# Kernel tuning notes

Measured on AMD Instinct MI355X. Metric: run time of the kernel, lower is better.

Reference implementation:

```python
import jax, jax.numpy as jnp
import numpy as np

# Module dims (match init_kwargs)
D_IN = 1024
N_PRI = 2048
D_PRI = 16
N_CLS = 25
D_CLS = 16
ITERS = 3
B = 64
EPS = 1e-6


def layer_norm(x, g, b, eps=1e-5):
    m = x.mean(-1, keepdims=True)
    v = ((x - m) ** 2).mean(-1, keepdims=True)
    return (x - m) / jnp.sqrt(v + eps) * g + b


def setup_inputs() -> dict:
    key = jax.random.key(0)
    ks = jax.random.split(key, 6)
    s = lambda n: 1.0 / np.sqrt(n)
    return {
        "z": jax.random.normal(ks[0], (B, D_IN), jnp.float32),
        # to_primary: Linear(d_in, n_primary*d_primary)
        "w1": jax.random.normal(ks[1], (D_IN, N_PRI * D_PRI), jnp.float32) * s(D_IN),
        "b1": jnp.zeros((N_PRI * D_PRI,), jnp.float32),
        # primary_act: LayerNorm(d_in) -> Linear(d_in, n_primary) -> Sigmoid
        "ln1_g": jnp.ones((D_IN,), jnp.float32),
        "ln1_b": jnp.zeros((D_IN,), jnp.float32),
        "w2": jax.random.normal(ks[2], (D_IN, N_PRI), jnp.float32) * s(D_IN),
        "b2": jnp.zeros((N_PRI,), jnp.float32),
        # CapsuleFC transform + EM routing params
        "w_caps": jax.random.normal(ks[3], (N_PRI, D_PRI, N_CLS, D_CLS), jnp.float32) * s(D_PRI),
        "beta_u": jnp.zeros((N_CLS,), jnp.float32),
        "beta_a": jnp.zeros((N_CLS,), jnp.float32),
        # to_logits: LayerNorm(d_class) -> Linear(d_class, 1)
        "ln2_g": jnp.ones((D_CLS,), jnp.float32),
        "ln2_b": jnp.zeros((D_CLS,), jnp.float32),
        "w3": jax.random.normal(ks[4], (D_CLS, 1), jnp.float32) * s(D_CLS),
        "b3": jnp.zeros((1,), jnp.float32),
    }


def em_routing(V, a_in, beta_u, beta_a, n_iter):
    # V: (b, n_in, n_out, d) votes; a_in: (b, n_in) primary activations
    b, n, o, d = V.shape
    R = jnp.full((b, n, o), 1.0 / o, V.dtype)  # routing assignments
    lam = jnp.asarray(1.0, V.dtype)            # inverse temperature
    for _ in range(n_iter):
        # M-step: weighted mean/variance per output capsule
        r = R * a_in[:, :, None]                                  # (b,n,o)
        r_sum = r.sum(axis=1) + EPS                               # (b,o)
        mu = jnp.einsum('bno,bnod->bod', r, V) / r_sum[..., None]  # (b,o,d)
        diff2 = (V - mu[:, None]) ** 2                            # (b,n,o,d)
        sigma2 = jnp.einsum('bno,bnod->bod', r, diff2) / r_sum[..., None] + EPS
        cost = (beta_u[None, :, None] + 0.5 * jnp.log(sigma2)) * r_sum[..., None]
        a_out = jax.nn.sigmoid(lam * (beta_a[None, :] - cost.sum(-1)))  # (b,o)
        # E-step: Gaussian log-likelihood of each vote under each output capsule
        logp = (-0.5 * (diff2 / sigma2[:, None]).sum(-1)
                - 0.5 * jnp.log(sigma2).sum(-1)[:, None, :])      # (b,n,o)
        R = jax.nn.softmax(jnp.log(a_out + EPS)[:, None, :] + logp, axis=-1)
    return mu, a_out, R


def reference(z, w1, b1, ln1_g, ln1_b, w2, b2, w_caps, beta_u, beta_a,
              ln2_g, ln2_b, w3, b3):
    b = z.shape[0]
    # primary poses (no squash: use_squash_primary=False)
    primary_pose = (z @ w1 + b1).reshape(b, N_PRI, D_PRI)
    # primary activations
    primary_act = jnp.clip(jax.nn.sigmoid(layer_norm(z, ln1_g, ln1_b) @ w2 + b2), 0.0, 1.0)
    # votes: each primary capsule predicts each class capsule's pose
    V = jnp.einsum('bni,niod->bnod', primary_pose, w_caps)  # (B, N_PRI, N_CLS, D_CLS)
    class_pose, class_act, q = em_routing(V, primary_act, beta_u, beta_a, ITERS)
    logits = (layer_norm(class_pose, ln2_g, ln2_b) @ w3 + b3).squeeze(-1)  # (B, N_CLS)
    acts = jnp.linalg.norm(class_pose, axis=-1)                            # (B, N_CLS)
    return logits, acts, class_pose, q
```

## Files before the change

### kernel.cpp

```cpp
#include <hip/hip_runtime.h>
#include <hip/hip_bf16.h>
#include <cstdio>

#define B     64
#define DIN   1024
#define NPRI  2048
#define DPRI  16
#define NCLS  25
#define DCLS  16
#define EMEPS 1e-6f
#define LNEPS 1e-5f
#define KS2   8
#define NCH   16

#define OFF_POSE 0
#define OFF_ZN   (OFF_POSE + NPRI*DPRI*B)
#define OFF_ACTT (OFF_ZN + B*DIN)
#define OFF_G2P  (OFF_ACTT + NPRI*B)
#define OFF_V    (OFF_G2P + KS2*NPRI*B)
#define V_FLOATS (NPRI*NCLS*B*DCLS/2)
#define OFF_R    (OFF_V + V_FLOATS)
#define R_FLOATS (NPRI*NCLS*B/2)
#define OFF_PART (OFF_R + R_FLOATS)
#define OFF_MU   (OFF_PART + NCLS*NCH*33*B)
#define OFF_MI4  (OFF_MU + NCLS*DCLS*B)
#define OFF_BASE (OFF_MI4 + NCLS*8*B*4)
#define OFF_ZH   (OFF_BASE + NCLS*B)
#define WS_FLOATS (OFF_ZH + B*DIN/2)

typedef __attribute__((ext_vector_type(8))) _Float16 f16x8;
typedef __attribute__((ext_vector_type(4))) float f32x4;

__device__ __forceinline__ unsigned pack_f16(float a, float b) {
  union { _Float16 h[2]; unsigned u; } x;
  x.h[0] = (_Float16)a; x.h[1] = (_Float16)b;
  return x.u;
}
__device__ __forceinline__ float f16lo(unsigned u) {
  union { unsigned u; _Float16 h[2]; } x; x.u = u; return (float)x.h[0];
}
__device__ __forceinline__ float f16hi(unsigned u) {
  union { unsigned u; _Float16 h[2]; } x; x.u = u; return (float)x.h[1];
}
__device__ __forceinline__ unsigned short f16bits(float a) {
  union { _Float16 h; unsigned short u; } x; x.h = (_Float16)a; return x.u;
}
__device__ __forceinline__ float f16val(unsigned short u) {
  union { unsigned short u; _Float16 h; } x; x.u = u; return (float)x.h;
}

__global__ __launch_bounds__(256) void k_lnzh(const float* __restrict__ z,
                                              const float* __restrict__ g,
                                              const float* __restrict__ bb,
                                              float* __restrict__ zn,
                                              unsigned* __restrict__ zh) {
  int row = blockIdx.x, t = threadIdx.x;
  const float* zr = z + row * DIN;
  float4 v = ((const float4*)zr)[t];
  uint2 hz = {pack_f16(v.x, v.y), pack_f16(v.z, v.w)};
  *(uint2*)&zh[row * 512 + t * 2] = hz;
  float s  = v.x + v.y + v.z + v.w;
  float s2 = v.x*v.x + v.y*v.y + v.z*v.z + v.w*v.w;
  for (int off = 32; off; off >>= 1) {
    s  += __shfl_down(s, off);
    s2 += __shfl_down(s2, off);
  }
  __shared__ float ls[8];
  int wv = t >> 6, ln = t & 63;
  if (ln == 0) { ls[wv*2] = s; ls[wv*2+1] = s2; }
  __syncthreads();
  s  = ls[0] + ls[2] + ls[4] + ls[6];
  s2 = ls[1] + ls[3] + ls[5] + ls[7];
  float mean = s * (1.0f / DIN);
  float var  = s2 * (1.0f / DIN) - mean * mean;
  float inv  = 1.0f / sqrtf(var + LNEPS);
  float4 gg = ((const float4*)g)[t];
  float4 bv = ((const float4*)bb)[t];
  float4 o;
  o.x = (v.x - mean) * inv * gg.x + bv.x;
  o.y = (v.y - mean) * inv * gg.y + bv.y;
  o.z = (v.z - mean) * inv * gg.z + bv.z;
  o.w = (v.w - mean) * inv * gg.w + bv.w;
  ((float4*)(zn + row * DIN))[t] = o;
}

__global__ __launch_bounds__(512) void k_gemm1m(const unsigned* __restrict__ zh,
                                                const float* __restrict__ w1,
                                                const float* __restrict__ b1,
                                                float* __restrict__ poseT) {
  __shared__ __align__(16) unsigned bt[2][64 * 68];
  __shared__ __align__(16) unsigned zl[2][64 * 68];
  int t = threadIdx.x;
  int c0 = blockIdx.x * 64;
  int l = t & 63, w = t >> 6;
  int kh = w >> 2, cw = w & 3;
  int c15 = l & 15, kq = l >> 4;
  int h  = t >> 8;
  int th = t & 255;
  int s_kp = th >> 2;
  int s_q  = th & 3;

  f32x4 acc0 = {0,0,0,0}, acc1 = {0,0,0,0}, acc2 = {0,0,0,0}, acc3 = {0,0,0,0};

  for (int it = 0; it < 4; ++it) {
    int k0 = (h * 4 + it) * 128;
#pragma unroll
    for (int u = 0; u < 4; ++u) {
      int cq = s_q + 4 * u;
      const float* src0 = w1 + (size_t)(k0 + 2 * s_kp) * 32768 + c0 + cq * 4;
      float4 r0 = *(const float4*)src0;
      float4 r1 = *(const float4*)(src0 + 32768);
      unsigned* dst = &bt[h][(cq * 4) * 68 + s_kp];
      dst[0]   = pack_f16(r0.x, r1.x);
      dst[68]  = pack_f16(r0.y, r1.y);
      dst[136] = pack_f16(r0.z, r1.z);
      dst[204] = pack_f16(r0.w, r1.w);
    }
#pragma unroll
    for (int u = 0; u < 4; ++u) {
      int ku4 = s_q + 4 * u;
      uint4 v = *(const uint4*)&zh[(size_t)s_kp * 512 + (k0 >> 1) + ku4 * 4];
      *(uint4*)&zl[h][s_kp * 68 + ku4 * 4] = v;
    }
    __syncthreads();
#pragma unroll
    for (int ks = 0; ks < 4; ++ks) {
      union { uint4 u; f16x8 hh; } bf, a0, a1, a2, a3;
      bf.u = *(const uint4*)&bt[kh][(cw * 16 + c15) * 68 + ks * 16 + kq * 4];
      a0.u = *(const uint4*)&zl[kh][(c15)      * 68 + ks * 16 + kq * 4];
      a1.u = *(const uint4*)&zl[kh][(16 + c15) * 68 + ks * 16 + kq * 4];
      a2.u = *(const uint4*)&zl[kh][(32 + c15) * 68 + ks * 16 + kq * 4];
      a3.u = *(const uint4*)&zl[kh][(48 + c15) * 68 + ks * 16 + kq * 4];
      acc0 = __builtin_amdgcn_mfma_f32_16x16x32_f16(a0.hh, bf.hh, acc0, 0, 0, 0);
      acc1 = __builtin_amdgcn_mfma_f32_16x16x32_f16(a1.hh, bf.hh, acc1, 0, 0, 0);
      acc2 = __builtin_amdgcn_mfma_f32_16x16x32_f16(a2.hh, bf.hh, acc2, 0, 0, 0);
      acc3 = __builtin_amdgcn_mfma_f32_16x16x32_f16(a3.hh, bf.hh, acc3, 0, 0, 0);
    }
    __syncthreads();
  }

  float* red = (float*)&zl[0][0];
  if (kh == 1) {
    int cc = cw * 16 + c15;
    *(float4*)&red[cc * 68 + kq * 4]      = *(float4*)&acc0;
    *(float4*)&red[cc * 68 + 16 + kq * 4] = *(float4*)&acc1;
    *(float4*)&red[cc * 68 + 32 + kq * 4] = *(float4*)&acc2;
    *(float4*)&red[cc * 68 + 48 + kq * 4] = *(float4*)&acc3;
  }
  __syncthreads();
  if (kh == 0) {
    int cc = cw * 16 + c15;
    int c = c0 + cc;
    float bc = b1[c];
    float4 r0 = *(float4*)&red[cc * 68 + kq * 4];
    float4 r1 = *(float4*)&red[cc * 68 + 16 + kq * 4];
    float4 r2 = *(float4*)&red[cc * 68 + 32 + kq * 4];
    float4 r3 = *(float4*)&red[cc * 68 + 48 + kq * 4];
    float* pdst = poseT + (size_t)c * 64 + kq * 4;
    float4 o0 = {acc0[0] + r0.x + bc, acc0[1] + r0.y + bc, acc0[2] + r0.z + bc, acc0[3] + r0.w + bc};
    float4 o1 = {acc1[0] + r1.x + bc, acc1[1] + r1.y + bc, acc1[2] + r1.z + bc, acc1[3] + r1.w + bc};
    float4 o2 = {acc2[0] + r2.x + bc, acc2[1] + r2.y + bc, acc2[2] + r2.z + bc, acc2[3] + r2.w + bc};
    float4 o3 = {acc3[0] + r3.x + bc, acc3[1] + r3.y + bc, acc3[2] + r3.z + bc, acc3[3] + r3.w + bc};
    *(float4*)&pdst[0]  = o0;
    *(float4*)&pdst[16] = o1;
    *(float4*)&pdst[32] = o2;
    *(float4*)&pdst[48] = o3;
  }
}

__global__ __launch_bounds__(256, 2) void k_gemm2p(const float* __restrict__ zn,
                                                   const float* __restrict__ w2,
                                                   float* __restrict__ part) {
  __shared__ __align__(16) float znT[128 * 68];
  __shared__ __align__(16) float wl[128 * 68];
  int t = threadIdx.x;
  int c0 = blockIdx.x * 64;
  int k0 = blockIdx.y * 128;
  int zr_ = t >> 2, za = t & 3;
  int wk = t >> 1, wc = (t & 1) * 32;

#pragma unroll
  for (int jj = 0; jj < 4; ++jj) {
    int kb = za * 8 + jj * 32;
    const float* src = zn + zr_ * DIN + k0 + kb;
    float4 v0 = *(const float4*)src;
    float4 v1 = *(const float4*)(src + 4);
    znT[(kb+0)*68 + zr_] = v0.x; znT[(kb+1)*68 + zr_] = v0.y;
    znT[(kb+2)*68 + zr_] = v0.z; znT[(kb+3)*68 + zr_] = v0.w;
    znT[(kb+4)*68 + zr_] = v1.x; znT[(kb+5)*68 + zr_] = v1.y;
    znT[(kb+6)*68 + zr_] = v1.z; znT[(kb+7)*68 + zr_] = v1.w;
  }
  const float* wsrc = w2 + (size_t)(k0 + wk) * NPRI + c0 + wc;
#pragma unroll
  for (int j = 0; j < 8; ++j)
    *(float4*)&wl[wk * 68 + wc + j * 4] = *(const float4*)(wsrc + j * 4);
  __syncthreads();

  int r0 = (t >> 4) * 4, c0l = (t & 15) * 4;
  float acc[4][4];
#pragma unroll
  for (int j = 0; j < 4; ++j)
#pragma unroll
    for (int i = 0; i < 4; ++i) acc[j][i] = 0.f;

#pragma unroll 4
  for (int k = 0; k < 128; ++k) {
    float4 z4 = *(const float4*)&znT[k * 68 + r0];
    float4 w4 = *(const float4*)&wl[k * 68 + c0l];
    float zz[4] = {z4.x, z4.y, z4.z, z4.w};
    float ww[4] = {w4.x, w4.y, w4.z, w4.w};
#pragma unroll
    for (int j = 0; j < 4; ++j)
#pragma unroll
      for (int i = 0; i < 4; ++i) acc[j][i] += ww[j] * zz[i];
  }
  float* pdst = part + ((size_t)blockIdx.y * NPRI + c0 + c0l) * 64 + r0;
#pragma unroll
  for (int j = 0; j < 4; ++j) {
    float4 o = {acc[j][0], acc[j][1], acc[j][2], acc[j][3]};
    *(float4*)&pdst[j * 64] = o;
  }
}

__global__ __launch_bounds__(256) void k_gemm2r(const float* __restrict__ part,
                                                const float* __restrict__ b2,
                                                float* __restrict__ actt) {
  int idx = blockIdx.x * 256 + threadIdx.x;
  float4 s = {0.f, 0.f, 0.f, 0.f};
#pragma unroll
  for (int kz = 0; kz < KS2; ++kz) {
    float4 v = *(const float4*)&part[(size_t)kz * NPRI * 64 + idx * 4];
    s.x += v.x; s.y += v.y; s.z += v.z; s.w += v.w;
  }
  int c = (idx * 4) >> 6;
  float bc = b2[c];
  float4 o;
  o.x = fminf(fmaxf(1.0f / (1.0f + expf(-(s.x + bc))), 0.0f), 1.0f);
  o.y = fminf(fmaxf(1.0f / (1.0f + expf(-(s.y + bc))), 0.0f), 1.0f);
  o.z = fminf(fmaxf(1.0f / (1.0f + expf(-(s.z + bc))), 0.0f), 1.0f);
  o.w = fminf(fmaxf(1.0f / (1.0f + expf(-(s.w + bc))), 0.0f), 1.0f);
  *(float4*)&actt[idx * 4] = o;
}

__global__ __launch_bounds__(256) void k_votes(const float* __restrict__ poseT,
                                               const float* __restrict__ wcaps,
                                               unsigned* __restrict__ V) {
  __shared__ __align__(16) float wl[6400];
  __shared__ __align__(16) float pl[64 * 16];
  int n = blockIdx.x, t = threadIdx.x;
  const float* wsrc = wcaps + (size_t)n * 6400;
  for (int idx = t * 4; idx < 6400; idx += 1024)
    *(float4*)(wl + idx) = *(const float4*)(wsrc + idx);
  {
    float4 v = *(const float4*)(poseT + n * 1024 + t * 4);
    int i = (t * 4) >> 6, b = (t * 4) & 63;
    pl[(b+0)*16 + i] = v.x; pl[(b+1)*16 + i] = v.y;
    pl[(b+2)*16 + i] = v.z; pl[(b+3)*16 + i] = v.w;
  }
  __syncthreads();
  if (t >= 200) return;
  int o = t / 8, d0 = (t % 8) * 2;
  float w0[16], w1_[16];
#pragma unroll
  for (int i = 0; i < 16; ++i) {
    w0[i]  = wl[(i * 25 + o) * 16 + d0];
    w1_[i] = wl[(i * 25 + o) * 16 + d0 + 1];
  }
  unsigned* vd = V + (((size_t)n * 25 + o) * 64 * 16 + d0) / 2;
  for (int b = 0; b < 64; ++b) {
    const float* pb = &pl[b * 16];
    float a0 = 0.f, a1 = 0.f;
#pragma unroll
    for (int i = 0; i < 16; ++i) {
      float p = pb[i];
      a0 += p * w0[i];
      a1 += p * w1_[i];
    }
    vd[b * 8] = pack_f16(a0, a1);
  }
}

template <bool UNIFORM>
__global__ __launch_bounds__(256) void k_stats(const unsigned* __restrict__ V,
                                               const float* __restrict__ actt,
                                               const unsigned short* __restrict__ Rh,
                                               float* __restrict__ part) {
  int o = blockIdx.y;
  int t = threadIdx.x, b = t & 63, wv = t >> 6;
  float S0 = 0.f, S1[16], S2[16];
#pragma unroll
  for (int d = 0; d < 16; ++d) { S1[d] = 0.f; S2[d] = 0.f; }
  int n0 = blockIdx.x * 128 + wv * 32;
  for (int k = 0; k < 32; ++k) {
    int n = n0 + k;
    float a = actt[n * 64 + b];
    float r = UNIFORM ? a * (1.0f / 25.0f)
                      : f16val(Rh[((size_t)n * 25 + o) * 64 + b]) * a;
    const uint4* vp = (const uint4*)(V + (((size_t)n * 25 + o) * 64 + b) * 8);
    uint4 u0 = vp[0], u1 = vp[1];
    unsigned uu[8] = {u0.x, u0.y, u0.z, u0.w, u1.x, u1.y, u1.z, u1.w};
    S0 += r;
#pragma unroll
    for (int q = 0; q < 8; ++q) {
      float v0 = f16lo(uu[q]), v1 = f16hi(uu[q]);
      float t0 = r * v0, t1 = r * v1;
      S1[2*q]   += t0;          S1[2*q+1] += t1;
      S2[2*q]   += t0 * v0;     S2[2*q+1] += t1 * v1;
    }
  }
  __shared__ float red[4 * 33 * 64];
  red[(wv * 33 + 0) * 64 + b] = S0;
#pragma unroll
  for (int d = 0; d < 16; ++d) {
    red[(wv * 33 + 1 + d) * 64 + b]  = S1[d];
    red[(wv * 33 + 17 + d) * 64 + b] = S2[d];
  }
  __syncthreads();
  if (wv == 0) {
    for (int s = 0; s < 33; ++s) {
      float tot = red[s * 64 + b] + red[(33 + s) * 64 + b] +
                  red[(66 + s) * 64 + b] + red[(99 + s) * 64 + b];
      part[((o * NCH + blockIdx.x) * 33 + s) * 64 + b] = tot;
    }
  }
}

template <bool FINAL>
__global__ __launch_bounds__(256) void k_redfin(const float* __restrict__ part,
                                                const float* __restrict__ beta_u,
                                                const float* __restrict__ beta_a,
                                                float* __restrict__ mi4,
                                                float* __restrict__ basew,
                                                const float* __restrict__ g2,
                                                const float* __restrict__ bb2,
                                                const float* __restrict__ w3,
                                                const float* __restrict__ b3,
                                                float* __restrict__ out) {
  __shared__ float st[33 * 64];
  int o = blockIdx.x, t = threadIdx.x;
  for (int slot = t; slot < 33 * 64; slot += 256) {
    float s = 0.f;
    const float* pp = part + (size_t)o * NCH * 2112 + slot;
#pragma unroll
    for (int c = 0; c < NCH; ++c) s += pp[(size_t)c * 2112];
    st[slot] = s;
  }
  __syncthreads();
  if (t < 64) {
    int b = t;
    float s0 = st[b];
    float rsm = s0 + EMEPS;
    float inv_rs = 1.0f / rsm;
    float ldet = 0.f;
    float mloc[16], iloc[16];
#pragma unroll
    for (int d = 0; d < 16; ++d) {
      float s1 = st[(1 + d) * 64 + b];
      float s2 = st[(17 + d) * 64 + b];
      float m = s1 * inv_rs;
      float var = (s2 - 2.0f * m * s1 + m * m * s0) * inv_rs;
      float sg = fmaxf(var, 0.0f) + EMEPS;
      mloc[d] = m;
      iloc[d] = 1.0f / sg;
      ldet += logf(sg);
    }
#pragma unroll
    for (int q = 0; q < 8; ++q) {
      float4 v = {mloc[2*q], iloc[2*q], mloc[2*q+1], iloc[2*q+1]};
      *(float4*)&mi4[((o * 8 + q) * 64 + b) * 4] = v;
    }
    float cost = (16.0f * beta_u[o] + 0.5f * ldet) * rsm;
    float x = beta_a[o] - cost;
    float a = 1.0f / (1.0f + expf(-x));
    basew[o * 64 + b] = logf(a + EMEPS) - 0.5f * ldet;

    if (FINAL) {
      float sm = 0.f;
#pragma unroll
      for (int d = 0; d < 16; ++d) sm += mloc[d];
      float mean = sm * (1.0f / 16.0f);
      float var2 = 0.f;
#pragma unroll
      for (int d = 0; d < 16; ++d) { float dd = mloc[d] - mean; var2 += dd * dd; }
      var2 *= (1.0f / 16.0f);
      float inv2 = 1.0f / sqrtf(var2 + LNEPS);
      float logit = 0.f, nrm = 0.f;
#pragma unroll
      for (int d = 0; d < 16; ++d) {
        float nh = (mloc[d] - mean) * inv2 * g2[d] + bb2[d];
        logit += nh * w3[d];
        nrm += mloc[d] * mloc[d];
      }
      out[b * 25 + o] = logit + b3[0];
      out[1600 + b * 25 + o] = sqrtf(nrm);
      float* pp = out + 3200 + (b * 25 + o) * 16;
#pragma unroll
      for (int d = 0; d < 16; ++d) pp[d] = mloc[d];
    }
  }
}

template <bool FINAL>
__global__ __launch_bounds__(256) void k_estep(const unsigned* __restrict__ V,
                                               const float* __restrict__ mi4,
                                               const float* __restrict__ basew,
                                               unsigned short* __restrict__ Rh,
                                               float* __restrict__ qout) {
  int t = threadIdx.x, b = t & 63, ng = t >> 6;
  int n = blockIdx.x * 4 + ng;
  float l[25];
  float mx = -1e30f;
#pragma unroll
  for (int o = 0; o < 25; ++o) {
    const uint4* vp = (const uint4*)(V + (((size_t)n * 25 + o) * 64 + b) * 8);
    uint4 u0 = vp[0], u1 = vp[1];
    unsigned uu[8] = {u0.x, u0.y, u0.z, u0.w, u1.x, u1.y, u1.z, u1.w};
    float acc = 0.f;
#pragma unroll
    for (int qq = 0; qq < 8; ++qq) {
      float4 mi = *(const float4*)&mi4[((o * 8 + qq) * 64 + b) * 4];
      float d0 = f16lo(uu[qq]) - mi.x;
      float d1 = f16hi(uu[qq]) - mi.z;
      acc += d0 * d0 * mi.y + d1 * d1 * mi.w;
    }
    l[o] = basew[o * 64 + b] - 0.5f * acc;
    mx = fmaxf(mx, l[o]);
  }
  float s = 0.f;
#pragma unroll
  for (int o = 0; o < 25; ++o) { l[o] = expf(l[o] - mx); s += l[o]; }
  float inv = 1.0f / s;
  if (FINAL) {
    float* qp = qout + ((size_t)b * NPRI + n) * 25;
#pragma unroll
    for (int o = 0; o < 25; ++o) qp[o] = l[o] * inv;
  } else {
#pragma unroll
    for (int o = 0; o < 25; ++o)
      Rh[((size_t)n * 25 + o) * 64 + b] = f16bits(l[o] * inv);
  }
}

extern "C" void kernel_launch(void* const* d_in, const int* in_sizes, int n_in,
                              void* d_out, int out_size, void* d_ws, size_t ws_size,
                              hipStream_t stream) {
  const float* z      = (const float*)d_in[0];
  const float* w1     = (const float*)d_in[1];
  const float* b1     = (const float*)d_in[2];
  const float* ln1g   = (const float*)d_in[3];
  const float* ln1b   = (const float*)d_in[4];
  const float* w2     = (const float*)d_in[5];
  const float* b2     = (const float*)d_in[6];
  const float* wcaps  = (const float*)d_in[7];
  const float* beta_u = (const float*)d_in[8];
  const float* beta_a = (const float*)d_in[9];
  const float* ln2g   = (const float*)d_in[10];
  const float* ln2b   = (const float*)d_in[11];
  const float* w3     = (const float*)d_in[12];
  const float* b3     = (const float*)d_in[13];

  if (ws_size < (size_t)WS_FLOATS * 4) {
    fprintf(stderr, "kernel_launch: ws too small: %zu < %zu bytes\n",
            ws_size, (size_t)WS_FLOATS * 4);
  }

  float* ws    = (float*)d_ws;
  float* out   = (float*)d_out;
  float* poseT = ws + OFF_POSE;
  float* zn    = ws + OFF_ZN;
  float* actt  = ws + OFF_ACTT;
  float* g2p   = ws + OFF_G2P;
  unsigned* V  = (unsigned*)(ws + OFF_V);
  unsigned short* Rh = (unsigned short*)(ws + OFF_R);
  float* part  = ws + OFF_PART;
  float* mi4   = ws + OFF_MI4;
  float* bse   = ws + OFF_BASE;
  unsigned* zh = (unsigned*)(ws + OFF_ZH);

  k_lnzh<<<64, 256, 0, stream>>>(z, ln1g, ln1b, zn, zh);
  k_gemm1m<<<512, 512, 0, stream>>>(zh, w1, b1, poseT);
  k_gemm2p<<<dim3(32, KS2), 256, 0, stream>>>(zn, w2, g2p);
  k_gemm2r<<<128, 256, 0, stream>>>(g2p, b2, actt);
  k_votes<<<2048, 256, 0, stream>>>(poseT, wcaps, V);

  k_stats<true><<<dim3(NCH, 25), 256, 0, stream>>>(V, actt, Rh, part);
  k_redfin<false><<<25, 256, 0, stream>>>(part, beta_u, beta_a, mi4, bse,
                                          ln2g, ln2b, w3, b3, out);

  k_estep<false><<<512, 256, 0, stream>>>(V, mi4, bse, Rh, nullptr);
  k_stats<false><<<dim3(NCH, 25), 256, 0, stream>>>(V, actt, Rh, part);
  k_redfin<false><<<25, 256, 0, stream>>>(part, beta_u, beta_a, mi4, bse,
                                          ln2g, ln2b, w3, b3, out);

  k_estep<false><<<512, 256, 0, stream>>>(V, mi4, bse, Rh, nullptr);
  k_stats<false><<<dim3(NCH, 25), 256, 0, stream>>>(V, actt, Rh, part);
  k_redfin<true><<<25, 256, 0, stream>>>(part, beta_u, beta_a, mi4, bse,
                                         ln2g, ln2b, w3, b3, out);

  k_estep<true><<<512, 256, 0, stream>>>(V, mi4, bse, nullptr, out + 28800);
}
```

Baseline: 350.0 us.

## Split GEMM1 K-halves across blocks and fold partial sum and bias into votes

The first projection GEMM moves from one 512-thread block that reduces two K-halves in shared memory to two 256-thread blocks per column tile, one per K-half, each writing its own partial pose buffer. The votes kernel then adds the two partials plus the bias while staging poses into shared memory. This doubles the number of blocks and halves shared memory per block to raise occupancy and parallelism on the weight-streaming GEMM, and drops the in-block reduction. In exchange it writes and reads an extra pose-sized partial buffer in global memory.

```diff
diff --git a/kernel.cpp b/kernel.cpp
--- a/kernel.cpp
+++ b/kernel.cpp
@@ -14,7 +14,7 @@
 #define NCH   16
 
 #define OFF_POSE 0
-#define OFF_ZN   (OFF_POSE + NPRI*DPRI*B)
+#define OFF_ZN   (OFF_POSE + 2*NPRI*DPRI*B)
 #define OFF_ACTT (OFF_ZN + B*DIN)
 #define OFF_G2P  (OFF_ACTT + NPRI*B)
 #define OFF_V    (OFF_G2P + KS2*NPRI*B)
@@ -22,8 +22,7 @@
 #define OFF_R    (OFF_V + V_FLOATS)
 #define R_FLOATS (NPRI*NCLS*B/2)
 #define OFF_PART (OFF_R + R_FLOATS)
-#define OFF_MU   (OFF_PART + NCLS*NCH*33*B)
-#define OFF_MI4  (OFF_MU + NCLS*DCLS*B)
+#define OFF_MI4  (OFF_PART + NCLS*NCH*33*B)
 #define OFF_BASE (OFF_MI4 + NCLS*8*B*4)
 #define OFF_ZH   (OFF_BASE + NCLS*B)
 #define WS_FLOATS (OFF_ZH + B*DIN/2)
@@ -84,33 +83,31 @@
   ((float4*)(zn + row * DIN))[t] = o;
 }
 
-__global__ __launch_bounds__(512) void k_gemm1m(const unsigned* __restrict__ zh,
+__global__ __launch_bounds__(256) void k_gemm1m(const unsigned* __restrict__ zh,
                                                 const float* __restrict__ w1,
-                                                const float* __restrict__ b1,
-                                                float* __restrict__ poseT) {
-  __shared__ __align__(16) unsigned bt[2][64 * 68];
-  __shared__ __align__(16) unsigned zl[2][64 * 68];
+                                                float* __restrict__ poseP) {
+  __shared__ __align__(16) unsigned bt[64 * 68];
+  __shared__ __align__(16) unsigned zl[64 * 68];
   int t = threadIdx.x;
   int c0 = blockIdx.x * 64;
-  int l = t & 63, w = t >> 6;
-  int kh = w >> 2, cw = w & 3;
+  int kh = blockIdx.y;
+  int l = t & 63, cw = t >> 6;
   int c15 = l & 15, kq = l >> 4;
-  int h  = t >> 8;
-  int th = t & 255;
-  int s_kp = th >> 2;
-  int s_q  = th & 3;
+  int s_kp = t >> 2;
+  int s_q  = t & 3;
 
   f32x4 acc0 = {0,0,0,0}, acc1 = {0,0,0,0}, acc2 = {0,0,0,0}, acc3 = {0,0,0,0};
 
   for (int it = 0; it < 4; ++it) {
-    int k0 = (h * 4 + it) * 128;
+    int k0 = (kh * 4 + it) * 128;
+    if (it) __syncthreads();
 #pragma unroll
     for (int u = 0; u < 4; ++u) {
       int cq = s_q + 4 * u;
       const float* src0 = w1 + (size_t)(k0 + 2 * s_kp) * 32768 + c0 + cq * 4;
       float4 r0 = *(const float4*)src0;
       float4 r1 = *(const float4*)(src0 + 32768);
-      unsigned* dst = &bt[h][(cq * 4) * 68 + s_kp];
+      unsigned* dst = &bt[(cq * 4) * 68 + s_kp];
       dst[0]   = pack_f16(r0.x, r1.x);
       dst[68]  = pack_f16(r0.y, r1.y);
       dst[136] = pack_f16(r0.z, r1.z);
@@ -120,52 +117,30 @@
     for (int u = 0; u < 4; ++u) {
       int ku4 = s_q + 4 * u;
       uint4 v = *(const uint4*)&zh[(size_t)s_kp * 512 + (k0 >> 1) + ku4 * 4];
-      *(uint4*)&zl[h][s_kp * 68 + ku4 * 4] = v;
+      *(uint4*)&zl[s_kp * 68 + ku4 * 4] = v;
     }
     __syncthreads();
 #pragma unroll
     for (int ks = 0; ks < 4; ++ks) {
       union { uint4 u; f16x8 hh; } bf, a0, a1, a2, a3;
-      bf.u = *(const uint4*)&bt[kh][(cw * 16 + c15) * 68 + ks * 16 + kq * 4];
-      a0.u = *(const uint4*)&zl[kh][(c15)      * 68 + ks * 16 + kq * 4];
-      a1.u = *(const uint4*)&zl[kh][(16 + c15) * 68 + ks * 16 + kq * 4];
-      a2.u = *(const uint4*)&zl[kh][(32 + c15) * 68 + ks * 16 + kq * 4];
-      a3.u = *(const uint4*)&zl[kh][(48 + c15) * 68 + ks * 16 + kq * 4];
+      bf.u = *(const uint4*)&bt[(cw * 16 + c15) * 68 + ks * 16 + kq * 4];
+      a0.u = *(const uint4*)&zl[(c15)      * 68 + ks * 16 + kq * 4];
+      a1.u = *(const uint4*)&zl[(16 + c15) * 68 + ks * 16 + kq * 4];
+      a2.u = *(const uint4*)&zl[(32 + c15) * 68 + ks * 16 + kq * 4];
+      a3.u = *(const uint4*)&zl[(48 + c15) * 68 + ks * 16 + kq * 4];
       acc0 = __builtin_amdgcn_mfma_f32_16x16x32_f16(a0.hh, bf.hh, acc0, 0, 0, 0);
       acc1 = __builtin_amdgcn_mfma_f32_16x16x32_f16(a1.hh, bf.hh, acc1, 0, 0, 0);
       acc2 = __builtin_amdgcn_mfma_f32_16x16x32_f16(a2.hh, bf.hh, acc2, 0, 0, 0);
       acc3 = __builtin_amdgcn_mfma_f32_16x16x32_f16(a3.hh, bf.hh, acc3, 0, 0, 0);
     }
-    __syncthreads();
-  }
-
-  float* red = (float*)&zl[0][0];
-  if (kh == 1) {
-    int cc = cw * 16 + c15;
-    *(float4*)&red[cc * 68 + kq * 4]      = *(float4*)&acc0;
-    *(float4*)&red[cc * 68 + 16 + kq * 4] = *(float4*)&acc1;
-    *(float4*)&red[cc * 68 + 32 + kq * 4] = *(float4*)&acc2;
-    *(float4*)&red[cc * 68 + 48 + kq * 4] = *(float4*)&acc3;
-  }
-  __syncthreads();
-  if (kh == 0) {
-    int cc = cw * 16 + c15;
-    int c = c0 + cc;
-    float bc = b1[c];
-    float4 r0 = *(float4*)&red[cc * 68 + kq * 4];
-    float4 r1 = *(float4*)&red[cc * 68 + 16 + kq * 4];
-    float4 r2 = *(float4*)&red[cc * 68 + 32 + kq * 4];
-    float4 r3 = *(float4*)&red[cc * 68 + 48 + kq * 4];
-    float* pdst = poseT + (size_t)c * 64 + kq * 4;
-    float4 o0 = {acc0[0] + r0.x + bc, acc0[1] + r0.y + bc, acc0[2] + r0.z + bc, acc0[3] + r0.w + bc};
-    float4 o1 = {acc1[0] + r1.x + bc, acc1[1] + r1.y + bc, acc1[2] + r1.z + bc, acc1[3] + r1.w + bc};
-    float4 o2 = {acc2[0] + r2.x + bc, acc2[1] + r2.y + bc, acc2[2] + r2.z + bc, acc2[3] + r2.w + bc};
-    float4 o3 = {acc3[0] + r3.x + bc, acc3[1] + r3.y + bc, acc3[2] + r3.z + bc, acc3[3] + r3.w + bc};
-    *(float4*)&pdst[0]  = o0;
-    *(float4*)&pdst[16] = o1;
-    *(float4*)&pdst[32] = o2;
-    *(float4*)&pdst[48] = o3;
-  }
+  }
+
+  int c = c0 + cw * 16 + c15;
+  float* pdst = poseP + (size_t)kh * (NPRI * DPRI * B) + (size_t)c * 64 + kq * 4;
+  *(float4*)&pdst[0]  = *(float4*)&acc0;
+  *(float4*)&pdst[16] = *(float4*)&acc1;
+  *(float4*)&pdst[32] = *(float4*)&acc2;
+  *(float4*)&pdst[48] = *(float4*)&acc3;
 }
 
 __global__ __launch_bounds__(256, 2) void k_gemm2p(const float* __restrict__ zn,
@@ -242,7 +217,8 @@
   *(float4*)&actt[idx * 4] = o;
 }
 
-__global__ __launch_bounds__(256) void k_votes(const float* __restrict__ poseT,
+__global__ __launch_bounds__(256) void k_votes(const float* __restrict__ poseP,
+                                               const float* __restrict__ b1,
                                                const float* __restrict__ wcaps,
                                                unsigned* __restrict__ V) {
   __shared__ __align__(16) float wl[6400];
@@ -252,10 +228,14 @@
   for (int idx = t * 4; idx < 6400; idx += 1024)
     *(float4*)(wl + idx) = *(const float4*)(wsrc + idx);
   {
-    float4 v = *(const float4*)(poseT + n * 1024 + t * 4);
-    int i = (t * 4) >> 6, b = (t * 4) & 63;
-    pl[(b+0)*16 + i] = v.x; pl[(b+1)*16 + i] = v.y;
-    pl[(b+2)*16 + i] = v.z; pl[(b+3)*16 + i] = v.w;
+    float4 v0 = *(const float4*)(poseP + n * 1024 + t * 4);
+    float4 v1 = *(const float4*)(poseP + (NPRI * DPRI * B) + n * 1024 + t * 4);
+    int i = t >> 4, b = (t & 15) * 4;
+    float bc_ = b1[n * 16 + i];
+    pl[(b+0)*16 + i] = v0.x + v1.x + bc_;
+    pl[(b+1)*16 + i] = v0.y + v1.y + bc_;
+    pl[(b+2)*16 + i] = v0.z + v1.z + bc_;
+    pl[(b+3)*16 + i] = v0.w + v1.w + bc_;
   }
   __syncthreads();
   if (t >= 200) return;
@@ -466,7 +446,7 @@
 
   float* ws    = (float*)d_ws;
   float* out   = (float*)d_out;
-  float* poseT = ws + OFF_POSE;
+  float* poseP = ws + OFF_POSE;
   float* zn    = ws + OFF_ZN;
   float* actt  = ws + OFF_ACTT;
   float* g2p   = ws + OFF_G2P;
@@ -478,10 +458,10 @@
   unsigned* zh = (unsigned*)(ws + OFF_ZH);
 
   k_lnzh<<<64, 256, 0, stream>>>(z, ln1g, ln1b, zn, zh);
-  k_gemm1m<<<512, 512, 0, stream>>>(zh, w1, b1, poseT);
+  k_gemm1m<<<dim3(512, 2), 256, 0, stream>>>(zh, w1, poseP);
   k_gemm2p<<<dim3(32, KS2), 256, 0, stream>>>(zn, w2, g2p);
   k_gemm2r<<<128, 256, 0, stream>>>(g2p, b2, actt);
-  k_votes<<<2048, 256, 0, stream>>>(poseT, wcaps, V);
+  k_votes<<<2048, 256, 0, stream>>>(poseP, b1, wcaps, V);
 
   k_stats<true><<<dim3(NCH, 25), 256, 0, stream>>>(V, actt, Rh, part);
   k_redfin<false><<<25, 256, 0, stream>>>(part, beta_u, beta_a, mi4, bse,
```

Result: no change. 350.0 us (-0.0%).
